# Kernel tuning notes

Hardware: AMD Instinct MI355X
Metric: run time of the kernel (lower is better)

The kernel has to match this reference:

```python
import jax, jax.numpy as jnp
import numpy as np

B, CIN, COUT, H, P, N = 8, 2, 1, 64, 16, 1024


def setup_inputs() -> dict:
    key = jax.random.key(0)
    ks = jax.random.split(key, 13)
    scale = 1.0 / (H * H)  # matches scale = 1/(in_channels*out_channels) of the layer
    return {
        "x": jax.random.normal(ks[0], (B, CIN, N), jnp.float32),
        "W0": jax.random.normal(ks[1], (CIN, H), jnp.float32) * 0.1,
        "b0": jnp.zeros((H,), jnp.float32),
        "wp": scale * jax.random.uniform(ks[2], (H, H, P), jnp.float32),
        "wpi": scale * jax.random.uniform(ks[3], (H, H, P), jnp.float32),
        "wr": scale * jax.random.uniform(ks[4], (H, H, P), jnp.float32),
        "wri": scale * jax.random.uniform(ks[5], (H, H, P), jnp.float32),
        "Wl": jax.random.normal(ks[6], (H, H), jnp.float32) * (1.0 / np.sqrt(H)),
        "bl": jnp.zeros((H,), jnp.float32),
        "W1": jax.random.normal(ks[7], (H, H), jnp.float32) * (1.0 / np.sqrt(H)),
        "b1": jnp.zeros((H,), jnp.float32),
        "W2": jax.random.normal(ks[8], (H, COUT), jnp.float32) * (1.0 / np.sqrt(H)),
        "b2": jnp.zeros((COUT,), jnp.float32),
    }


def reference(x, W0, b0, wp, wpi, wr, wri, Wl, bl, W1, b1, W2, b2):
    # Lift: StandardMLP([CIN, H]) = single Linear, applied channels-last
    h = jnp.einsum("bcn,ch->bhn", x, W0) + b0[None, :, None]  # (B,H,N)

    # LaplaceLayer
    poles = wp + 1j * wpi          # (H,H,P) complex64
    residues = wr + 1j * wri       # (H,H,P)
    alpha = jnp.fft.fft(h)         # (B,H,N) complex64
    # lambda_k = 2*pi*i*fftfreq(N, dt=1/N) -> 2*pi*i*integer frequencies
    lam = (jnp.fft.fftfreq(N, 1.0 / N) * (2.0 * jnp.pi) * 1j).astype(jnp.complex64)
    # Cauchy transfer kernel H(s) = res / (s - pole): (N, i, o, p)
    Hw = residues[None, :, :, :] / (lam[:, None, None, None] - poles[None, :, :, :])
    out_res1 = jnp.einsum("bin,niop->bon", alpha, Hw)   # steady-state residues (B,H,N)
    out_res2 = -jnp.einsum("bin,niop->bop", alpha, Hw)  # transient residues (B,H,P)
    x1 = jnp.fft.ifft(out_res1, n=N).real               # (B,H,N)
    t = jnp.linspace(0.0, 1.0, N).astype(jnp.complex64)
    exp_term = jnp.exp(poles[:, :, :, None] * t)        # (i,o,p,n)
    x2 = jnp.einsum("bop,iopn->bon", out_res2, exp_term).real / N
    skip = jnp.einsum("bin,io->bon", h, Wl) + bl[None, :, None]
    h = jax.nn.gelu(x1 + x2 + skip)                     # activation after layer

    # Project: Linear -> gelu -> Linear (channels-last), back to channels-first
    z = jax.nn.gelu(jnp.einsum("bhn,hk->bkn", h, W1) + b1[None, :, None])
    out = jnp.einsum("bkn,ko->bon", z, W2) + b2[None, :, None]
    return out  # (B, COUT, N)
```

## Files before the change

kernel.cpp:

```cpp
#include <hip/hip_runtime.h>
#include <math.h>

#define NN 1024
#define PD 16

__device__ __forceinline__ float gelu_tanh(float x) {
    float x3 = x * x * x;
    float inner = 0.7978845608028654f * (x + 0.044715f * x3);
    return 0.5f * x * (1.0f + tanhf(inner));
}

#define PADI(i) ((i) + ((i) >> 4))

#define WAVE_FENCE() asm volatile("" ::: "memory")

__device__ __forceinline__ void bf_dif(float2* A, const float2* tw, int i0, int i1, int ti) {
    float2 a = A[PADI(i0)];
    float2 b = A[PADI(i1)];
    float2 c = tw[ti];
    float dx = a.x - b.x, dy = a.y - b.y;
    A[PADI(i0)] = make_float2(a.x + b.x, a.y + b.y);
    A[PADI(i1)] = make_float2(dx * c.x - dy * c.y, dx * c.y + dy * c.x);
}

__device__ __forceinline__ void bf_dit(float2* A, const float2* tw, int i0, int i1, int ti) {
    float2 a = A[PADI(i0)];
    float2 b = A[PADI(i1)];
    float2 c = tw[ti];
    float tx = b.x * c.x + b.y * c.y;
    float ty = b.y * c.x - b.x * c.y;
    A[PADI(i0)] = make_float2(a.x + tx, a.y + ty);
    A[PADI(i1)] = make_float2(a.x - tx, a.y - ty);
}

__device__ __forceinline__ void dit_wave_stages(float2* A, const float2* tw, int lane, int cb) {
#pragma unroll
    for (int s = 1; s <= 8; ++s) {
        int m = 1 << s, half = m >> 1;
#pragma unroll
        for (int k = 0; k < 2; ++k) {
            int lb = lane + k * 64;
            int grp = lb >> (s - 1), pos = lb & (half - 1);
            int i0 = cb + grp * m + pos;
            bf_dit(A, tw, i0, i0 + half, pos << (10 - s));
        }
        WAVE_FENCE();
    }
}

__device__ __forceinline__ void dit_cross_stages(float2* A, const float2* tw, int tid) {
    __syncthreads();
#pragma unroll
    for (int k = 0; k < 2; ++k) {
        int w = tid + k * 256;
        int grp = w >> 8, pos = w & 255;
        int i0 = grp * 512 + pos;
        bf_dit(A, tw, i0, i0 + 256, pos << 1);
    }
    __syncthreads();
#pragma unroll
    for (int k = 0; k < 2; ++k) {
        int w = tid + k * 256;
        bf_dit(A, tw, w, w + 512, w);
    }
    __syncthreads();
}

__global__ __launch_bounds__(256) void k_main(const float* __restrict__ x,
                                              const float* __restrict__ W0,
                                              const float* __restrict__ b0,
                                              float* __restrict__ u1, float* __restrict__ u2,
                                              float* __restrict__ alpha0,
                                              float* __restrict__ A1v, float* __restrict__ A2v) {
    __shared__ float2 A[NN + (NN >> 4)];
    __shared__ float2 S[NN];
    __shared__ float2 tw[512];
    int bi = blockIdx.x;
    int b = bi >> 6, i = bi & 63;
    int tid = threadIdx.x;
    int lane = tid & 63, wv = tid >> 6, cb = wv << 8;
    int n0 = tid * 4;

    float w00 = W0[i], w01 = W0[64 + i], b0i = b0[i];
    {
        const float4* x0v = (const float4*)(x + b * 2048);
        const float4* x1v = (const float4*)(x + b * 2048 + 1024);
        float4 v0 = x0v[tid];
        float4 v1 = x1v[tid];
        A[PADI(n0 + 0)] = make_float2(v0.x * w00 + v1.x * w01 + b0i, 0.f);
        A[PADI(n0 + 1)] = make_float2(v0.y * w00 + v1.y * w01 + b0i, 0.f);
        A[PADI(n0 + 2)] = make_float2(v0.z * w00 + v1.z * w01 + b0i, 0.f);
        A[PADI(n0 + 3)] = make_float2(v0.w * w00 + v1.w * w01 + b0i, 0.f);
    }
    for (int j = tid; j < 512; j += 256) {
        float sn, cs;
        sincosf(-6.283185307179586f * (float)j * (1.0f / 1024.0f), &sn, &cs);
        tw[j] = make_float2(cs, sn);
    }
    __syncthreads();

#pragma unroll
    for (int k = 0; k < 2; ++k) {
        int w = tid + k * 256;
        bf_dif(A, tw, w, w + 512, w);
    }
    __syncthreads();
#pragma unroll
    for (int k = 0; k < 2; ++k) {
        int w = tid + k * 256;
        int grp = w >> 8, pos = w & 255;
        int i0 = grp * 512 + pos;
        bf_dif(A, tw, i0, i0 + 256, pos << 1);
    }
    __syncthreads();
#pragma unroll
    for (int s = 8; s >= 1; --s) {
        int m = 1 << s, half = m >> 1;
#pragma unroll
        for (int k = 0; k < 2; ++k) {
            int lb = lane + k * 64;
            int grp = lb >> (s - 1), pos = lb & (half - 1);
            int i0 = cb + grp * m + pos;
            bf_dif(A, tw, i0, i0 + half, pos << (10 - s));
        }
        WAVE_FENCE();
    }

    {
#pragma unroll
        for (int j = 0; j < 4; ++j) {
            int r = n0 + j;
            float2 a = A[PADI(r)];
            S[r] = a;
            if (r == 0) alpha0[bi] = a.x;
            int fj = (int)(__brev((unsigned)r) >> 22);
            float2 v;
            if (fj == 0) {
                v = make_float2(0.f, 0.f);
            } else {
                float f = (fj < 512) ? (float)fj : (float)(fj - 1024);
                float wq = 6.283185307179586f * f;
                v = make_float2(a.y / wq, -a.x / wq);
            }
            A[PADI(r)] = v;
        }
    }
    WAVE_FENCE();

    dit_wave_stages(A, tw, lane, cb);
    dit_cross_stages(A, tw, tid);

    const float invN = 1.0f / (float)NN;
    {
        float2 a0 = A[PADI(n0 + 0)];
        float2 a1 = A[PADI(n0 + 1)];
        float2 a2 = A[PADI(n0 + 2)];
        float2 a3 = A[PADI(n0 + 3)];
        ((float4*)(u1 + bi * NN))[tid] = make_float4(a0.x * invN, a1.x * invN, a2.x * invN, a3.x * invN);
        if (tid == 0) A1v[bi] = a0.x;
#pragma unroll
        for (int j = 0; j < 4; ++j) {
            int r = n0 + j;
            int fj = (int)(__brev((unsigned)r) >> 22);
            float2 v;
            if (fj == 0) {
                v = make_float2(0.f, 0.f);
            } else {
                float f = (fj < 512) ? (float)fj : (float)(fj - 1024);
                float g = -1.0f / (39.47841760435743f * f * f);
                float2 s = S[r];
                v = make_float2(s.x * g, s.y * g);
            }
            A[PADI(r)] = v;
        }
    }
    WAVE_FENCE();

    dit_wave_stages(A, tw, lane, cb);
    dit_cross_stages(A, tw, tid);

    {
        float2 a0 = A[PADI(n0 + 0)];
        float2 a1 = A[PADI(n0 + 1)];
        float2 a2 = A[PADI(n0 + 2)];
        float2 a3 = A[PADI(n0 + 3)];
        ((float4*)(u2 + bi * NN))[tid] = make_float4(a0.x * invN, a1.x * invN, a2.x * invN, a3.x * invN);
        if (tid == 0) A2v[bi] = a0.x;
    }
}

__global__ __launch_bounds__(256) void k_small(const float* __restrict__ wp,
                                               const float* __restrict__ wpi,
                                               const float* __restrict__ wr,
                                               const float* __restrict__ wri,
                                               const float* __restrict__ alpha0,
                                               const float* __restrict__ A1v,
                                               const float* __restrict__ A2v,
                                               float* __restrict__ WA, float* __restrict__ WB,
                                               float* __restrict__ c0, float* __restrict__ c1,
                                               float* __restrict__ c2) {
    __shared__ float a0s[512], a1s[512], a2s[512];
    __shared__ float wred[4][16][28];
    int o = blockIdx.x;
    int tid = threadIdx.x;
    int p = tid & 15;
    int i4 = tid >> 4;
    for (int t = tid; t < 512; t += 256) {
        a0s[t] = alpha0[t];
        a1s[t] = A1v[t];
        a2s[t] = A2v[t];
    }
    __syncthreads();

    float p1x = 0.f, p1y = 0.f, p2x = 0.f, p2y = 0.f;
    float r2x[8], r2y[8], t0[8];
#pragma unroll
    for (int b = 0; b < 8; ++b) { r2x[b] = 0.f; r2y[b] = 0.f; t0[b] = 0.f; }
    float rrs[4], rpxs[4];

#pragma unroll
    for (int ib = 0; ib < 4; ++ib) {
        int i = ib * 16 + i4;
        int idx = (i * 64 + o) * PD + p;
        float rr = wr[idx], ri = wri[idx], pr = wp[idx], pim = wpi[idx];
        float inv = 1.0f / (pr * pr + pim * pim);
        float ripx = (rr * pr + ri * pim) * inv;
        float ripy = (ri * pr - rr * pim) * inv;
        float rpx = rr * pr - ri * pim;
        float rpy = rr * pim + ri * pr;
        rrs[ib] = rr;
        rpxs[ib] = rpx;
        p1x += pr; p1y += pim;
        p2x += pr * pr - pim * pim;
        p2y += 2.0f * pr * pim;
#pragma unroll
        for (int b = 0; b < 8; ++b) {
            float a1 = a1s[b * 64 + i], a2 = a2s[b * 64 + i], a0 = a0s[b * 64 + i];
            r2x[b] += -rr * a1 - rpx * a2 + ripx * a0;
            r2y[b] += -ri * a1 - rpy * a2 + ripy * a0;
            t0[b] += -a0 * ripx;
        }
    }

#pragma unroll
    for (int ib = 0; ib < 4; ++ib) {
        float wa = rrs[ib], wb = rpxs[ib];
        for (int off = 8; off >= 1; off >>= 1) {
            wa += __shfl_xor(wa, off);
            wb += __shfl_xor(wb, off);
        }
        if (p == 0) {
            int i = ib * 16 + i4;
            WA[i * 64 + o] = wa;
            WB[i * 64 + o] = wb;
        }
    }

    float q[28];
    q[0] = p1x; q[1] = p1y; q[2] = p2x; q[3] = p2y;
#pragma unroll
    for (int b = 0; b < 8; ++b) { q[4 + b] = r2x[b]; q[12 + b] = r2y[b]; q[20 + b] = t0[b]; }
#pragma unroll
    for (int k = 0; k < 28; ++k) {
        q[k] += __shfl_down(q[k], 32);
        q[k] += __shfl_down(q[k], 16);
    }
    int lane = tid & 63, wv = tid >> 6;
    if (lane < 16) {
#pragma unroll
        for (int k = 0; k < 28; ++k) wred[wv][lane][k] = q[k];
    }
    __syncthreads();
    if (tid < 16) {
        float s[28];
#pragma unroll
        for (int k = 0; k < 28; ++k)
            s[k] = wred[0][tid][k] + wred[1][tid][k] + wred[2][tid][k] + wred[3][tid][k];
        const float invN = 1.0f / 1024.0f;
        float cc[24];
#pragma unroll
        for (int b = 0; b < 8; ++b) {
            float rx = s[4 + b], ry = s[12 + b];
            cc[b] = (64.0f * rx + s[20 + b]) * invN;
            cc[8 + b] = (rx * s[0] - ry * s[1]) * invN;
            cc[16 + b] = (rx * s[2] - ry * s[3]) * (0.5f * invN);
        }
#pragma unroll
        for (int k = 0; k < 24; ++k) {
            cc[k] += __shfl_xor(cc[k], 1);
            cc[k] += __shfl_xor(cc[k], 2);
            cc[k] += __shfl_xor(cc[k], 4);
            cc[k] += __shfl_xor(cc[k], 8);
        }
        if (tid == 0) {
#pragma unroll
            for (int b = 0; b < 8; ++b) {
                c0[b * 64 + o] = cc[b];
                c1[b * 64 + o] = cc[8 + b];
                c2[b * 64 + o] = cc[16 + b];
            }
        }
    }
}

__global__ __launch_bounds__(256) void k_gout(const float* __restrict__ x,
                                              const float* __restrict__ W0,
                                              const float* __restrict__ b0,
                                              const float* __restrict__ u1,
                                              const float* __restrict__ u2,
                                              const float* __restrict__ WA,
                                              const float* __restrict__ WB,
                                              const float* __restrict__ Wl,
                                              const float* __restrict__ bl,
                                              const float* __restrict__ c0,
                                              const float* __restrict__ c1,
                                              const float* __restrict__ c2,
                                              const float* __restrict__ W1,
                                              const float* __restrict__ b1,
                                              const float* __restrict__ W2,
                                              const float* __restrict__ b2,
                                              float* __restrict__ out) {
    __shared__ float sU1[64 * 32], sU2[64 * 32];
    __shared__ float sWl[4096], sWA[4096], sWB[4096], sW1[4096];
    __shared__ float hhs[64 * 34];
    __shared__ float sW0a[64], sW0b[64], sb0[64], sbl[64];
    __shared__ float sc0[64], sc1[64], sc2[64], sb1[64], sW2[64];
    __shared__ float red[8 * 32];
    int tid = threadIdx.x;
    int b = blockIdx.x >> 5;
    int n0 = (blockIdx.x & 31) << 5;

    {
        const float4* Wl4 = (const float4*)Wl;
        const float4* WA4 = (const float4*)WA;
        const float4* WB4 = (const float4*)WB;
        const float4* W14 = (const float4*)W1;
        for (int j = tid; j < 1024; j += 256) {
            ((float4*)sWl)[j] = Wl4[j];
            ((float4*)sWA)[j] = WA4[j];
            ((float4*)sWB)[j] = WB4[j];
            ((float4*)sW1)[j] = W14[j];
        }
        const float4* u14 = (const float4*)u1;
        const float4* u24 = (const float4*)u2;
        int nb4 = n0 >> 2;
        for (int j = tid; j < 512; j += 256) {
            int i = j >> 3, c4 = j & 7;
            ((float4*)sU1)[j] = u14[(b * 64 + i) * 256 + nb4 + c4];
            ((float4*)sU2)[j] = u24[(b * 64 + i) * 256 + nb4 + c4];
        }
        if (tid < 64) {
            sW0a[tid] = W0[tid];
            sW0b[tid] = W0[64 + tid];
            sb0[tid] = b0[tid];
            sbl[tid] = bl[tid];
            sc0[tid] = c0[b * 64 + tid];
            sc1[tid] = c1[b * 64 + tid];
            sc2[tid] = c2[b * 64 + tid];
            sb1[tid] = b1[tid];
            sW2[tid] = W2[tid];
        }
    }
    __syncthreads();

    {
        int og = tid >> 4, ng = tid & 15;
        int oB = og * 4, nB = ng * 2;
        float x0a = x[b * 2048 + n0 + nB];
        float x0b = x[b * 2048 + n0 + nB + 1];
        float x1a = x[b * 2048 + 1024 + n0 + nB];
        float x1b = x[b * 2048 + 1024 + n0 + nB + 1];
        float acc0[4], acc1[4];
#pragma unroll
        for (int r = 0; r < 4; ++r) { acc0[r] = 0.f; acc1[r] = 0.f; }
        for (int i = 0; i < 64; ++i) {
            float w0a = sW0a[i], w0b = sW0b[i], bb = sb0[i];
            float hva = x0a * w0a + x1a * w0b + bb;
            float hvb = x0b * w0a + x1b * w0b + bb;
            float2 ua = *(const float2*)&sU1[i * 32 + nB];
            float2 va = *(const float2*)&sU2[i * 32 + nB];
            float4 wl = *(const float4*)&sWl[i * 64 + oB];
            float4 wa = *(const float4*)&sWA[i * 64 + oB];
            float4 wb = *(const float4*)&sWB[i * 64 + oB];
            acc0[0] += hva * wl.x + ua.x * wa.x + va.x * wb.x;
            acc1[0] += hvb * wl.x + ua.y * wa.x + va.y * wb.x;
            acc0[1] += hva * wl.y + ua.x * wa.y + va.x * wb.y;
            acc1[1] += hvb * wl.y + ua.y * wa.y + va.y * wb.y;
            acc0[2] += hva * wl.z + ua.x * wa.z + va.x * wb.z;
            acc1[2] += hvb * wl.z + ua.y * wa.z + va.y * wb.z;
            acc0[3] += hva * wl.w + ua.x * wa.w + va.x * wb.w;
            acc1[3] += hvb * wl.w + ua.y * wa.w + va.y * wb.w;
        }
        float ta = (float)(n0 + nB) * (1.0f / 1023.0f);
        float tb = (float)(n0 + nB + 1) * (1.0f / 1023.0f);
#pragma unroll
        for (int r = 0; r < 4; ++r) {
            int o = oB + r;
            float ga = acc0[r] + sbl[o] + sc0[o] + sc1[o] * ta + sc2[o] * ta * ta;
            float gb = acc1[r] + sbl[o] + sc0[o] + sc1[o] * tb + sc2[o] * tb * tb;
            hhs[o * 34 + nB] = gelu_tanh(ga);
            hhs[o * 34 + nB + 1] = gelu_tanh(gb);
        }
    }
    __syncthreads();

    {
        int n = tid & 31, kq = tid >> 5;
        float z[8];
#pragma unroll
        for (int k = 0; k < 8; ++k) z[k] = 0.f;
        for (int o = 0; o < 64; ++o) {
            float hv = hhs[o * 34 + n];
            float4 w1a = *(const float4*)&sW1[o * 64 + kq * 8];
            float4 w1b = *(const float4*)&sW1[o * 64 + kq * 8 + 4];
            z[0] += hv * w1a.x; z[1] += hv * w1a.y; z[2] += hv * w1a.z; z[3] += hv * w1a.w;
            z[4] += hv * w1b.x; z[5] += hv * w1b.y; z[6] += hv * w1b.z; z[7] += hv * w1b.w;
        }
        float part = 0.f;
#pragma unroll
        for (int k = 0; k < 8; ++k) part += gelu_tanh(z[k] + sb1[kq * 8 + k]) * sW2[kq * 8 + k];
        red[kq * 32 + n] = part;
    }
    __syncthreads();
    if (tid < 32) {
        float s = red[tid];
#pragma unroll
        for (int k = 1; k < 8; ++k) s += red[k * 32 + tid];
        out[b * 1024 + n0 + tid] = s + b2[0];
    }
}

extern "C" void kernel_launch(void* const* d_in, const int* in_sizes, int n_in,
                              void* d_out, int out_size, void* d_ws, size_t ws_size,
                              hipStream_t stream) {
    const float* x = (const float*)d_in[0];
    const float* W0 = (const float*)d_in[1];
    const float* b0 = (const float*)d_in[2];
    const float* wp = (const float*)d_in[3];
    const float* wpi = (const float*)d_in[4];
    const float* wr = (const float*)d_in[5];
    const float* wri = (const float*)d_in[6];
    const float* Wl = (const float*)d_in[7];
    const float* bl = (const float*)d_in[8];
    const float* W1 = (const float*)d_in[9];
    const float* b1 = (const float*)d_in[10];
    const float* W2 = (const float*)d_in[11];
    const float* b2 = (const float*)d_in[12];

    float* ws = (float*)d_ws;
    float* u1 = ws;
    float* u2 = ws + 524288;
    float* alpha0 = ws + 1048576;
    float* A1v = alpha0 + 512;
    float* A2v = alpha0 + 1024;
    float* c0 = alpha0 + 1536;
    float* c1 = alpha0 + 2048;
    float* c2 = alpha0 + 2560;
    float* WA = alpha0 + 3072;
    float* WB = alpha0 + 3072 + 4096;

    k_main<<<512, 256, 0, stream>>>(x, W0, b0, u1, u2, alpha0, A1v, A2v);
    k_small<<<64, 256, 0, stream>>>(wp, wpi, wr, wri, alpha0, A1v, A2v, WA, WB, c0, c1, c2);
    k_gout<<<256, 256, 0, stream>>>(x, W0, b0, u1, u2, WA, WB, Wl, bl, c0, c1, c2,
                                    W1, b1, W2, b2, (float*)d_out);
}
```

Before: 110.5 us.

## Pack two real channels per complex FFT and merge the two inverse FFTs

Each block now handles two channels by packing their real signals into one complex FFT, then splits the spectra using conjugate symmetry. The two inverse transforms (the 1/(iω) and -1/ω² filters) are combined into one complex spectrum per channel, with u1 in the real part and u2 in the imaginary part, and the two channels' inverse FFTs run interleaved. This halves the forward FFT count and the grid size, and replaces two serial inverse FFTs per channel with one. In exchange it uses more shared memory per block and launches only 256 blocks, which lowers parallelism.

```diff
diff --git a/kernel.cpp b/kernel.cpp
--- a/kernel.cpp
+++ b/kernel.cpp
@@ -33,7 +33,8 @@
     A[PADI(i1)] = make_float2(a.x - tx, a.y - ty);
 }
 
-__device__ __forceinline__ void dit_wave_stages(float2* A, const float2* tw, int lane, int cb) {
+__device__ __forceinline__ void dit_wave_dual(float2* A0, float2* A1, const float2* tw,
+                                              int lane, int cb) {
 #pragma unroll
     for (int s = 1; s <= 8; ++s) {
         int m = 1 << s, half = m >> 1;
@@ -42,26 +43,29 @@
             int lb = lane + k * 64;
             int grp = lb >> (s - 1), pos = lb & (half - 1);
             int i0 = cb + grp * m + pos;
-            bf_dit(A, tw, i0, i0 + half, pos << (10 - s));
+            int ti = pos << (10 - s);
+            bf_dit(A0, tw, i0, i0 + half, ti);
+            bf_dit(A1, tw, i0, i0 + half, ti);
         }
         WAVE_FENCE();
     }
 }
 
-__device__ __forceinline__ void dit_cross_stages(float2* A, const float2* tw, int tid) {
+__device__ __forceinline__ void dit_cross_dual(float2* A0, float2* A1, const float2* tw, int tid) {
     __syncthreads();
 #pragma unroll
     for (int k = 0; k < 2; ++k) {
         int w = tid + k * 256;
-        int grp = w >> 8, pos = w & 255;
-        int i0 = grp * 512 + pos;
-        bf_dit(A, tw, i0, i0 + 256, pos << 1);
+        int pos = w & 255, i0 = (w >> 8) * 512 + pos;
+        bf_dit(A0, tw, i0, i0 + 256, pos << 1);
+        bf_dit(A1, tw, i0, i0 + 256, pos << 1);
     }
     __syncthreads();
 #pragma unroll
     for (int k = 0; k < 2; ++k) {
         int w = tid + k * 256;
-        bf_dit(A, tw, w, w + 512, w);
+        bf_dit(A0, tw, w, w + 512, w);
+        bf_dit(A1, tw, w, w + 512, w);
     }
     __syncthreads();
 }
@@ -73,24 +77,32 @@
                                               float* __restrict__ alpha0,
                                               float* __restrict__ A1v, float* __restrict__ A2v) {
     __shared__ float2 A[NN + (NN >> 4)];
-    __shared__ float2 S[NN];
+    __shared__ float2 B[NN + (NN >> 4)];
+    __shared__ float2 Z[NN];
     __shared__ float2 tw[512];
-    int bi = blockIdx.x;
-    int b = bi >> 6, i = bi & 63;
+    int blk = blockIdx.x;
+    int bi0 = blk * 2, bi1 = bi0 + 1;
+    int b = bi0 >> 6;
+    int ia = bi0 & 63, ib = ia + 1;
     int tid = threadIdx.x;
     int lane = tid & 63, wv = tid >> 6, cb = wv << 8;
     int n0 = tid * 4;
 
-    float w00 = W0[i], w01 = W0[64 + i], b0i = b0[i];
+    float w00a = W0[ia], w01a = W0[64 + ia], b0a = b0[ia];
+    float w00b = W0[ib], w01b = W0[64 + ib], b0b = b0[ib];
     {
         const float4* x0v = (const float4*)(x + b * 2048);
         const float4* x1v = (const float4*)(x + b * 2048 + 1024);
         float4 v0 = x0v[tid];
         float4 v1 = x1v[tid];
-        A[PADI(n0 + 0)] = make_float2(v0.x * w00 + v1.x * w01 + b0i, 0.f);
-        A[PADI(n0 + 1)] = make_float2(v0.y * w00 + v1.y * w01 + b0i, 0.f);
-        A[PADI(n0 + 2)] = make_float2(v0.z * w00 + v1.z * w01 + b0i, 0.f);
-        A[PADI(n0 + 3)] = make_float2(v0.w * w00 + v1.w * w01 + b0i, 0.f);
+        float xe[4] = {v0.x, v0.y, v0.z, v0.w};
+        float xo[4] = {v1.x, v1.y, v1.z, v1.w};
+#pragma unroll
+        for (int j = 0; j < 4; ++j) {
+            float hA = xe[j] * w00a + xo[j] * w01a + b0a;
+            float hB = xe[j] * w00b + xo[j] * w01b + b0b;
+            A[PADI(n0 + j)] = make_float2(hA, hB);
+        }
     }
     for (int j = tid; j < 512; j += 256) {
         float sn, cs;
@@ -108,8 +120,7 @@
 #pragma unroll
     for (int k = 0; k < 2; ++k) {
         int w = tid + k * 256;
-        int grp = w >> 8, pos = w & 255;
-        int i0 = grp * 512 + pos;
+        int pos = w & 255, i0 = (w >> 8) * 512 + pos;
         bf_dif(A, tw, i0, i0 + 256, pos << 1);
     }
     __syncthreads();
@@ -126,66 +137,64 @@
         WAVE_FENCE();
     }
 
-    {
-#pragma unroll
-        for (int j = 0; j < 4; ++j) {
-            int r = n0 + j;
-            float2 a = A[PADI(r)];
-            S[r] = a;
-            if (r == 0) alpha0[bi] = a.x;
-            int fj = (int)(__brev((unsigned)r) >> 22);
-            float2 v;
-            if (fj == 0) {
-                v = make_float2(0.f, 0.f);
-            } else {
-                float f = (fj < 512) ? (float)fj : (float)(fj - 1024);
-                float wq = 6.283185307179586f * f;
-                v = make_float2(a.y / wq, -a.x / wq);
-            }
-            A[PADI(r)] = v;
+#pragma unroll
+    for (int j = 0; j < 4; ++j) {
+        int r = n0 + j;
+        Z[r] = A[PADI(r)];
+    }
+    if (tid == 0) {
+        alpha0[bi0] = Z[0].x;
+        alpha0[bi1] = Z[0].y;
+    }
+    __syncthreads();
+
+#pragma unroll
+    for (int j = 0; j < 4; ++j) {
+        int r = n0 + j;
+        int fj = (int)(__brev((unsigned)r) >> 22);
+        if (fj == 0) {
+            A[PADI(r)] = make_float2(0.f, 0.f);
+            B[PADI(r)] = make_float2(0.f, 0.f);
+        } else {
+            int jm = (NN - fj) & (NN - 1);
+            int rm = (int)(__brev((unsigned)jm) >> 22);
+            float2 Zk = Z[r];
+            float2 Zm = Z[rm];
+            float Cc = Zm.x, Dd = -Zm.y;
+            float aax = 0.5f * (Zk.x + Cc), aay = 0.5f * (Zk.y + Dd);
+            float abx = 0.5f * (Zk.y - Dd), aby = -0.5f * (Zk.x - Cc);
+            float f = (fj < 512) ? (float)fj : (float)(fj - 1024);
+            float w = 6.283185307179586f * f;
+            float q = 1.0f / w + 1.0f / (w * w);
+            A[PADI(r)] = make_float2(aay * q, -aax * q);
+            B[PADI(r)] = make_float2(aby * q, -abx * q);
         }
     }
     WAVE_FENCE();
 
-    dit_wave_stages(A, tw, lane, cb);
-    dit_cross_stages(A, tw, tid);
+    dit_wave_dual(A, B, tw, lane, cb);
+    dit_cross_dual(A, B, tw, tid);
 
     const float invN = 1.0f / (float)NN;
     {
-        float2 a0 = A[PADI(n0 + 0)];
-        float2 a1 = A[PADI(n0 + 1)];
-        float2 a2 = A[PADI(n0 + 2)];
-        float2 a3 = A[PADI(n0 + 3)];
-        ((float4*)(u1 + bi * NN))[tid] = make_float4(a0.x * invN, a1.x * invN, a2.x * invN, a3.x * invN);
-        if (tid == 0) A1v[bi] = a0.x;
-#pragma unroll
-        for (int j = 0; j < 4; ++j) {
-            int r = n0 + j;
-            int fj = (int)(__brev((unsigned)r) >> 22);
-            float2 v;
-            if (fj == 0) {
-                v = make_float2(0.f, 0.f);
-            } else {
-                float f = (fj < 512) ? (float)fj : (float)(fj - 1024);
-                float g = -1.0f / (39.47841760435743f * f * f);
-                float2 s = S[r];
-                v = make_float2(s.x * g, s.y * g);
-            }
-            A[PADI(r)] = v;
-        }
-    }
-    WAVE_FENCE();
-
-    dit_wave_stages(A, tw, lane, cb);
-    dit_cross_stages(A, tw, tid);
-
-    {
-        float2 a0 = A[PADI(n0 + 0)];
-        float2 a1 = A[PADI(n0 + 1)];
-        float2 a2 = A[PADI(n0 + 2)];
-        float2 a3 = A[PADI(n0 + 3)];
-        ((float4*)(u2 + bi * NN))[tid] = make_float4(a0.x * invN, a1.x * invN, a2.x * invN, a3.x * invN);
-        if (tid == 0) A2v[bi] = a0.x;
+        float2 a0 = A[PADI(n0 + 0)], a1 = A[PADI(n0 + 1)];
+        float2 a2 = A[PADI(n0 + 2)], a3 = A[PADI(n0 + 3)];
+        float2 bb0 = B[PADI(n0 + 0)], bb1 = B[PADI(n0 + 1)];
+        float2 bb2 = B[PADI(n0 + 2)], bb3 = B[PADI(n0 + 3)];
+        ((float4*)(u1 + bi0 * NN))[tid] =
+            make_float4(a0.x * invN, a1.x * invN, a2.x * invN, a3.x * invN);
+        ((float4*)(u2 + bi0 * NN))[tid] =
+            make_float4(a0.y * invN, a1.y * invN, a2.y * invN, a3.y * invN);
+        ((float4*)(u1 + bi1 * NN))[tid] =
+            make_float4(bb0.x * invN, bb1.x * invN, bb2.x * invN, bb3.x * invN);
+        ((float4*)(u2 + bi1 * NN))[tid] =
+            make_float4(bb0.y * invN, bb1.y * invN, bb2.y * invN, bb3.y * invN);
+        if (tid == 0) {
+            A1v[bi0] = a0.x;
+            A2v[bi0] = a0.y;
+            A1v[bi1] = bb0.x;
+            A2v[bi1] = bb0.y;
+        }
     }
 }
 
@@ -219,8 +228,8 @@
     float rrs[4], rpxs[4];
 
 #pragma unroll
-    for (int ib = 0; ib < 4; ++ib) {
-        int i = ib * 16 + i4;
+    for (int ibl = 0; ibl < 4; ++ibl) {
+        int i = ibl * 16 + i4;
         int idx = (i * 64 + o) * PD + p;
         float rr = wr[idx], ri = wri[idx], pr = wp[idx], pim = wpi[idx];
         float inv = 1.0f / (pr * pr + pim * pim);
@@ -228,8 +237,8 @@
         float ripy = (ri * pr - rr * pim) * inv;
         float rpx = rr * pr - ri * pim;
         float rpy = rr * pim + ri * pr;
-        rrs[ib] = rr;
-        rpxs[ib] = rpx;
+        rrs[ibl] = rr;
+        rpxs[ibl] = rpx;
         p1x += pr; p1y += pim;
         p2x += pr * pr - pim * pim;
         p2y += 2.0f * pr * pim;
@@ -243,14 +252,14 @@
     }
 
 #pragma unroll
-    for (int ib = 0; ib < 4; ++ib) {
-        float wa = rrs[ib], wb = rpxs[ib];
+    for (int ibl = 0; ibl < 4; ++ibl) {
+        float wa = rrs[ibl], wb = rpxs[ibl];
         for (int off = 8; off >= 1; off >>= 1) {
             wa += __shfl_xor(wa, off);
             wb += __shfl_xor(wb, off);
         }
         if (p == 0) {
-            int i = ib * 16 + i4;
+            int i = ibl * 16 + i4;
             WA[i * 64 + o] = wa;
             WB[i * 64 + o] = wb;
         }
@@ -418,7 +427,8 @@
         }
         float part = 0.f;
 #pragma unroll
-        for (int k = 0; k < 8; ++k) part += gelu_tanh(z[k] + sb1[kq * 8 + k]) * sW2[kq * 8 + k];
+        for (int k = 0; k < 8; ++k)
+            part += gelu_tanh(z[k] + sb1[kq * 8 + k]) * sW2[kq * 8 + k];
         red[kq * 32 + n] = part;
     }
     __syncthreads();
@@ -459,7 +469,7 @@
     float* WA = alpha0 + 3072;
     float* WB = alpha0 + 3072 + 4096;
 
-    k_main<<<512, 256, 0, stream>>>(x, W0, b0, u1, u2, alpha0, A1v, A2v);
+    k_main<<<256, 256, 0, stream>>>(x, W0, b0, u1, u2, alpha0, A1v, A2v);
     k_small<<<64, 256, 0, stream>>>(wp, wpi, wr, wri, alpha0, A1v, A2v, WA, WB, c0, c1, c2);
     k_gout<<<256, 256, 0, stream>>>(x, W0, b0, u1, u2, WA, WB, Wl, bl, c0, c1, c2,
                                     W1, b1, W2, b2, (float*)d_out);
```

Result: faster. 107.9 us (-2.4%).
